# Kernel optimization log

Hardware: AMD Instinct MI355X
Metric: run time of the kernel (lower is better)

The kernel has to match this reference:

```python
import jax, jax.numpy as jnp
import numpy as np

# ---- static dims ----
B, C, T, H, W = 8, 3, 2, 256, 256
P = 16
GH, GW = H // P, W // P          # 16, 16 patch grid
HW = GH * GW                      # 256 patches per frame
D = 512                           # model dim
HEADS, DH = 8, 64
INNER = HEADS * DH                # 512
FF = 4 * D
Q, K, L = 256, 1024, 1            # quant_dim, codebook_size, code_seq_len
DEPTH = 2                         # spatial/temporal depth
CPP = C * P * P                   # 768
SCALE = 1.0 / float(np.sqrt(DH))


def _ln(x, g, b):
    m = jnp.mean(x, -1, keepdims=True)
    v = jnp.mean(jnp.square(x - m), -1, keepdims=True)
    return (x - m) * jax.lax.rsqrt(v + 1e-5) * g + b


def _attn(x, wqkv, wo, bias):
    N, S, _ = x.shape
    q, k, v = jnp.split(x @ wqkv, 3, axis=-1)
    q = q.reshape(N, S, HEADS, DH)
    k = k.reshape(N, S, HEADS, DH)
    v = v.reshape(N, S, HEADS, DH)
    s = jnp.einsum('bihd,bjhd->bhij', q, k) * SCALE
    if bias is not None:
        s = s + bias
    a = jax.nn.softmax(s, -1)
    o = jnp.einsum('bhij,bjhd->bihd', a, v).reshape(N, S, INNER)
    return o @ wo


def _cross(x, ctx, wq, wkv, wo):
    N, S, _ = x.shape
    Lc = ctx.shape[1]
    q = (x @ wq).reshape(N, S, HEADS, DH)
    k, v = jnp.split(ctx @ wkv, 2, axis=-1)
    k = k.reshape(N, Lc, HEADS, DH)
    v = v.reshape(N, Lc, HEADS, DH)
    s = jnp.einsum('bihd,bjhd->bhij', q, k) * SCALE
    a = jax.nn.softmax(s, -1)
    o = jnp.einsum('bhij,bjhd->bihd', a, v).reshape(N, S, INNER)
    return o @ wo


def _self_tf(x, bias, params):
    def step(x, p):
        l1g, l1b, wqkv, wo, l2g, l2b, w1, b1, w2, b2 = p
        x = x + _attn(_ln(x, l1g, l1b), wqkv, wo, bias)
        x = x + jax.nn.gelu(_ln(x, l2g, l2b) @ w1 + b1) @ w2 + b2
        return x, None
    x, _ = jax.lax.scan(step, x, params)
    return x


def _dec_tf(x, bias, ctx, params):
    def step(x, p):
        l1g, l1b, wqkv, wo, cg, cbb, wq, wkv, cwo, l2g, l2b, w1, b1, w2, b2 = p
        x = x + _attn(_ln(x, l1g, l1b), wqkv, wo, bias)
        x = x + _cross(_ln(x, cg, cbb), ctx, wq, wkv, cwo)
        x = x + jax.nn.gelu(_ln(x, l2g, l2b) @ w1 + b1) @ w2 + b2
        return x, None
    x, _ = jax.lax.scan(step, x, params)
    return x


def _cpb(w1, b1, w2, b2):
    # continuous relative position bias over the patch grid -> [HEADS, HW, HW]
    yy, xx = jnp.meshgrid(jnp.arange(GH), jnp.arange(GW), indexing='ij')
    pos = jnp.stack([yy, xx], -1).reshape(HW, 2).astype(jnp.float32)
    rel = pos[:, None] - pos[None, :]
    bias = jax.nn.relu(rel @ w1 + b1) @ w2 + b2
    return jnp.transpose(bias, (2, 0, 1))


def _forward(video, pe_ln1g, pe_ln1b, pe_w, pe_b, pe_ln2g, pe_ln2b,
             cpb_w1, cpb_b1, cpb_w2, cpb_b2,
             es_ln1g, es_ln1b, es_wqkv, es_wo, es_ln2g, es_ln2b, es_w1, es_b1, es_w2, es_b2,
             et_ln1g, et_ln1b, et_wqkv, et_wo, et_ln2g, et_ln2b, et_w1, et_b1, et_w2, et_b2,
             ds_ln1g, ds_ln1b, ds_wqkv, ds_wo, ds_clng, ds_clnb, ds_wq, ds_wkv, ds_cwo,
             ds_ln2g, ds_ln2b, ds_w1, ds_b1, ds_w2, ds_b2,
             vq_inw, vq_inb, codebook, vq_outw, vq_outb, noise,
             px_w, px_b):
    # patch embed: b c t (h p1) (w p2) -> b t h w (c p1 p2), LN -> Linear -> LN
    x = video.reshape(B, C, T, GH, P, GW, P).transpose(0, 2, 3, 5, 1, 4, 6).reshape(B, T, GH, GW, CPP)
    x = _ln(x, pe_ln1g, pe_ln1b) @ pe_w + pe_b
    tokens = _ln(x, pe_ln2g, pe_ln2b)                      # [B, T, GH, GW, D]

    bias = _cpb(cpb_w1, cpb_b1, cpb_w2, cpb_b2)

    # encoder: spatial over (b t)(h w), temporal over (b h w) t
    sp = _self_tf(tokens.reshape(B * T, HW, D), bias,
                  (es_ln1g, es_ln1b, es_wqkv, es_wo, es_ln2g, es_ln2b, es_w1, es_b1, es_w2, es_b2))
    tm = sp.reshape(B, T, GH, GW, D).transpose(0, 2, 3, 1, 4).reshape(B * HW, T, D)
    tm = _self_tf(tm, None,
                  (et_ln1g, et_ln1b, et_wqkv, et_wo, et_ln2g, et_ln2b, et_w1, et_b1, et_w2, et_b2))
    tokens = tm.reshape(B, GH, GW, T, D).transpose(0, 3, 1, 2, 4)  # [B, T, GH, GW, D]

    # NSVQ bottleneck on the last-frame tokens
    feat = tokens[:, 1].reshape(B, HW, D).mean(1)          # [B, D]
    z = (feat @ vq_inw + vq_inb).reshape(B, L, Q)
    d2 = (jnp.sum(z * z, -1, keepdims=True)
          - 2.0 * jnp.einsum('blq,kq->blk', z, codebook)
          + jnp.sum(codebook * codebook, -1))              # [B, L, K]
    idx = jnp.argmin(d2, -1)                               # [B, L]
    hard = codebook[idx]                                   # gather codewords
    err = jnp.linalg.norm(z - hard, axis=-1, keepdims=True)
    zq = z + err / (jnp.linalg.norm(noise, axis=-1, keepdims=True) + 1e-8) * noise
    act = zq @ vq_outw + vq_outb                           # [B, L, D] action tokens

    # decoder: spatial transformer with cross-attn to quantized action tokens
    ctx = jnp.broadcast_to(act[:, None], (B, T, L, D)).reshape(B * T, L, D)
    dec = _dec_tf(tokens.reshape(B * T, HW, D), bias, ctx,
                  (ds_ln1g, ds_ln1b, ds_wqkv, ds_wo, ds_clng, ds_clnb, ds_wq, ds_wkv, ds_cwo,
                   ds_ln2g, ds_ln2b, ds_w1, ds_b1, ds_w2, ds_b2))
    pix = dec.reshape(B, T, GH, GW, D) @ px_w + px_b        # [B, T, GH, GW, CPP]
    recon = pix.reshape(B, T, GH, GW, C, P, P).transpose(0, 4, 1, 2, 5, 3, 6).reshape(B, C, T, H, W)
    return recon


def setup_inputs() -> dict:
    key = jax.random.key(0)
    ks = jax.random.split(key, 64)
    ctr = iter(range(64))
    def nrm(shape, s=0.02):
        return (jax.random.normal(ks[next(ctr)], shape) * s).astype(jnp.float32)
    ones = lambda sh: jnp.ones(sh, jnp.float32)
    zeros = lambda sh: jnp.zeros(sh, jnp.float32)
    inp = dict(
        video=jax.random.normal(ks[next(ctr)], (B, C, T, H, W), jnp.float32),
        pe_ln1g=ones((CPP,)), pe_ln1b=zeros((CPP,)), pe_w=nrm((CPP, D)), pe_b=zeros((D,)),
        pe_ln2g=ones((D,)), pe_ln2b=zeros((D,)),
        cpb_w1=nrm((2, D), 0.1), cpb_b1=zeros((D,)), cpb_w2=nrm((D, HEADS), 0.1), cpb_b2=zeros((HEADS,)),
        es_ln1g=ones((DEPTH, D)), es_ln1b=zeros((DEPTH, D)), es_wqkv=nrm((DEPTH, D, 3 * INNER)),
        es_wo=nrm((DEPTH, INNER, D)), es_ln2g=ones((DEPTH, D)), es_ln2b=zeros((DEPTH, D)),
        es_w1=nrm((DEPTH, D, FF)), es_b1=zeros((DEPTH, FF)), es_w2=nrm((DEPTH, FF, D)), es_b2=zeros((DEPTH, D)),
        et_ln1g=ones((DEPTH, D)), et_ln1b=zeros((DEPTH, D)), et_wqkv=nrm((DEPTH, D, 3 * INNER)),
        et_wo=nrm((DEPTH, INNER, D)), et_ln2g=ones((DEPTH, D)), et_ln2b=zeros((DEPTH, D)),
        et_w1=nrm((DEPTH, D, FF)), et_b1=zeros((DEPTH, FF)), et_w2=nrm((DEPTH, FF, D)), et_b2=zeros((DEPTH, D)),
        ds_ln1g=ones((DEPTH, D)), ds_ln1b=zeros((DEPTH, D)), ds_wqkv=nrm((DEPTH, D, 3 * INNER)),
        ds_wo=nrm((DEPTH, INNER, D)), ds_clng=ones((DEPTH, D)), ds_clnb=zeros((DEPTH, D)),
        ds_wq=nrm((DEPTH, D, INNER)), ds_wkv=nrm((DEPTH, D, 2 * INNER)), ds_cwo=nrm((DEPTH, INNER, D)),
        ds_ln2g=ones((DEPTH, D)), ds_ln2b=zeros((DEPTH, D)),
        ds_w1=nrm((DEPTH, D, FF)), ds_b1=zeros((DEPTH, FF)), ds_w2=nrm((DEPTH, FF, D)), ds_b2=zeros((DEPTH, D)),
        vq_inw=nrm((D, Q)), vq_inb=zeros((Q,)), codebook=nrm((K, Q), 0.05),
        vq_outw=nrm((Q, D)), vq_outb=zeros((D,)),
        noise=jax.random.normal(ks[next(ctr)], (B, L, Q), jnp.float32),
        px_w=nrm((D, CPP)), px_b=zeros((CPP,)),
    )
    return inp


def reference(video, pe_ln1g, pe_ln1b, pe_w, pe_b, pe_ln2g, pe_ln2b,
              cpb_w1, cpb_b1, cpb_w2, cpb_b2,
              es_ln1g, es_ln1b, es_wqkv, es_wo, es_ln2g, es_ln2b, es_w1, es_b1, es_w2, es_b2,
              et_ln1g, et_ln1b, et_wqkv, et_wo, et_ln2g, et_ln2b, et_w1, et_b1, et_w2, et_b2,
              ds_ln1g, ds_ln1b, ds_wqkv, ds_wo, ds_clng, ds_clnb, ds_wq, ds_wkv, ds_cwo,
              ds_ln2g, ds_ln2b, ds_w1, ds_b1, ds_w2, ds_b2,
              vq_inw, vq_inb, codebook, vq_outw, vq_outb, noise,
              px_w, px_b):
    return _forward(video, pe_ln1g, pe_ln1b, pe_w, pe_b, pe_ln2g, pe_ln2b,
                    cpb_w1, cpb_b1, cpb_w2, cpb_b2,
                    es_ln1g, es_ln1b, es_wqkv, es_wo, es_ln2g, es_ln2b, es_w1, es_b1, es_w2, es_b2,
                    et_ln1g, et_ln1b, et_wqkv, et_wo, et_ln2g, et_ln2b, et_w1, et_b1, et_w2, et_b2,
                    ds_ln1g, ds_ln1b, ds_wqkv, ds_wo, ds_clng, ds_clnb, ds_wq, ds_wkv, ds_cwo,
                    ds_ln2g, ds_ln2b, ds_w1, ds_b1, ds_w2, ds_b2,
                    vq_inw, vq_inb, codebook, vq_outw, vq_outb, noise,
                    px_w, px_b)
```

## Files before the change

### kernel.cpp

```cpp
#include <hip/hip_runtime.h>
#include <math.h>

#define SCALE 0.125f

typedef unsigned short u16;
typedef short s16x8 __attribute__((ext_vector_type(8)));
typedef u16 u16x8 __attribute__((ext_vector_type(8)));
typedef float f32x4 __attribute__((ext_vector_type(4)));

__device__ __forceinline__ float wred_sum(float v) {
#pragma unroll
  for (int o = 32; o; o >>= 1) v += __shfl_xor(v, o, 64);
  return v;
}
__device__ __forceinline__ float wred_max(float v) {
#pragma unroll
  for (int o = 32; o; o >>= 1) v = fmaxf(v, __shfl_xor(v, o, 64));
  return v;
}
__device__ __forceinline__ float gelu_tanh(float x) {
  float x3 = x * x * x;
  return 0.5f * x * (1.0f + tanhf(0.7978845608028654f * (x + 0.044715f * x3)));
}
__device__ __forceinline__ u16 f2bf(float f) {
  unsigned u = __float_as_uint(f);
  return (u16)((u + 0x7fffu + ((u >> 16) & 1u)) >> 16);
}

struct TP6 { const float* s0; const float* s1; const float* s2;
             const float* s3; const float* s4; const float* s5; };

__global__ __launch_bounds__(256) void wtrans_k(TP6 p, u16* __restrict__ dst,
                                                int K, int N, size_t mstride) {
  const float* srcs[6] = {p.s0, p.s1, p.s2, p.s3, p.s4, p.s5};
  const float* src = srcs[blockIdx.z];
  u16* d = dst + (size_t)blockIdx.z * mstride;
  __shared__ float t[32][33];
  const int tx = threadIdx.x, ty = threadIdx.y;
  const int n0 = blockIdx.x * 32, k0 = blockIdx.y * 32;
#pragma unroll
  for (int i = 0; i < 4; ++i) t[ty + i * 8][tx] = src[(size_t)(k0 + ty + i * 8) * N + n0 + tx];
  __syncthreads();
#pragma unroll
  for (int i = 0; i < 4; ++i)
    d[(size_t)(n0 + ty + i * 8) * K + k0 + tx] = f2bf(t[tx][ty + i * 8]);
}

template <bool GELU, bool BIAS, bool RES>
__global__ __launch_bounds__(256) void mgemm_k(const float* __restrict__ A,
                                               const u16* __restrict__ Bt,
                                               const float* __restrict__ bias,
                                               const float* __restrict__ res,
                                               float* __restrict__ C,
                                               int M, int N, int K) {
  __shared__ u16 As[128 * 64];
  __shared__ u16 Bs[128 * 64];
  const int tid = threadIdx.x;
  const int lane = tid & 63, wid = tid >> 6;
  const int wr = wid >> 1, wc = wid & 1;
  const int m0 = blockIdx.y * 128, n0 = blockIdx.x * 128;
  f32x4 acc[4][4];
#pragma unroll
  for (int m = 0; m < 4; ++m)
#pragma unroll
    for (int n = 0; n < 4; ++n) acc[m][n] = (f32x4){0.f, 0.f, 0.f, 0.f};

  for (int k0 = 0; k0 < K; k0 += 64) {
#pragma unroll
    for (int p = 0; p < 4; ++p) {
      const int i = p * 256 + tid;
      const int r = i >> 3, c8 = i & 7;
      const float4* src = (const float4*)&A[(size_t)(m0 + r) * K + k0 + c8 * 8];
      const float4 f0 = src[0], f1 = src[1];
      u16x8 h;
      h[0] = f2bf(f0.x); h[1] = f2bf(f0.y); h[2] = f2bf(f0.z); h[3] = f2bf(f0.w);
      h[4] = f2bf(f1.x); h[5] = f2bf(f1.y); h[6] = f2bf(f1.z); h[7] = f2bf(f1.w);
      const int byte = r * 128 + ((c8 * 16) ^ ((r & 7) << 4));
      *(u16x8*)((char*)As + byte) = h;
    }
#pragma unroll
    for (int p = 0; p < 4; ++p) {
      const int i = p * 256 + tid;
      const int r = i >> 3, c = i & 7;
      const u16x8 h = *(const u16x8*)&Bt[(size_t)(n0 + r) * K + k0 + c * 8];
      const int byte = r * 128 + ((c * 16) ^ ((r & 7) << 4));
      *(u16x8*)((char*)Bs + byte) = h;
    }
    __syncthreads();
#pragma unroll
    for (int ks = 0; ks < 2; ++ks) {
      const int kb = ks * 64 + ((lane >> 4) << 4);
      s16x8 af[4], bfr[4];
#pragma unroll
      for (int m = 0; m < 4; ++m) {
        const int r = wr * 64 + m * 16 + (lane & 15);
        af[m] = *(const s16x8*)((const char*)As + r * 128 + (kb ^ ((r & 7) << 4)));
      }
#pragma unroll
      for (int n = 0; n < 4; ++n) {
        const int r = wc * 64 + n * 16 + (lane & 15);
        bfr[n] = *(const s16x8*)((const char*)Bs + r * 128 + (kb ^ ((r & 7) << 4)));
      }
#pragma unroll
      for (int m = 0; m < 4; ++m)
#pragma unroll
        for (int n = 0; n < 4; ++n)
          acc[m][n] = __builtin_amdgcn_mfma_f32_16x16x32_bf16(af[m], bfr[n], acc[m][n], 0, 0, 0);
    }
    __syncthreads();
  }
#pragma unroll
  for (int m = 0; m < 4; ++m) {
    const int row = m0 + wr * 64 + m * 16 + ((lane >> 4) << 2);
#pragma unroll
    for (int n = 0; n < 4; ++n) {
      const int col = n0 + wc * 64 + n * 16 + (lane & 15);
      const float bs = BIAS ? bias[col] : 0.0f;
#pragma unroll
      for (int j = 0; j < 4; ++j) {
        float v = acc[m][n][j] + bs;
        if (GELU) v = gelu_tanh(v);
        if (RES) v += res[(size_t)(row + j) * N + col];
        C[(size_t)(row + j) * N + col] = v;
      }
    }
  }
}

static void mgemm(hipStream_t st, const float* A, const u16* Bt, const float* bias,
                  const float* res, float* C, int M, int N, int K, bool gelu) {
  dim3 g(N / 128, M / 128);
  if (gelu)
    mgemm_k<true, true, false><<<g, 256, 0, st>>>(A, Bt, bias, res, C, M, N, K);
  else if (bias && res)
    mgemm_k<false, true, true><<<g, 256, 0, st>>>(A, Bt, bias, res, C, M, N, K);
  else if (bias)
    mgemm_k<false, true, false><<<g, 256, 0, st>>>(A, Bt, bias, res, C, M, N, K);
  else if (res)
    mgemm_k<false, false, true><<<g, 256, 0, st>>>(A, Bt, bias, res, C, M, N, K);
  else
    mgemm_k<false, false, false><<<g, 256, 0, st>>>(A, Bt, bias, res, C, M, N, K);
}

__global__ __launch_bounds__(256) void pembed_k(const float* __restrict__ video,
                                                const float* __restrict__ g,
                                                const float* __restrict__ b,
                                                float* __restrict__ xpe) {
  const int row = blockIdx.x;
  const int gw_ = row & 15, gh_ = (row >> 4) & 15, t = (row >> 8) & 1, bb = row >> 9;
  const int tid = threadIdx.x;
  float v[3];
  float s = 0.f, ss = 0.f;
#pragma unroll
  for (int r = 0; r < 3; ++r) {
    const int e = tid + r * 256;
    const int c = e >> 8, rem = e & 255, p1 = rem >> 4, p2 = rem & 15;
    v[r] = video[((size_t)(((bb * 3 + c) * 2 + t) * 256 + gh_ * 16 + p1)) * 256 + gw_ * 16 + p2];
    s += v[r];
    ss += v[r] * v[r];
  }
  __shared__ float r1[4], r2[4];
  s = wred_sum(s);
  ss = wred_sum(ss);
  if ((tid & 63) == 0) { r1[tid >> 6] = s; r2[tid >> 6] = ss; }
  __syncthreads();
  const float S = r1[0] + r1[1] + r1[2] + r1[3];
  const float SS = r2[0] + r2[1] + r2[2] + r2[3];
  const float mean = S * (1.0f / 768.0f);
  const float var = SS * (1.0f / 768.0f) - mean * mean;
  const float inv = rsqrtf(var + 1e-5f);
  float* out = xpe + (size_t)row * 768;
#pragma unroll
  for (int r = 0; r < 3; ++r) {
    const int e = tid + r * 256;
    out[e] = (v[r] - mean) * inv * g[e] + b[e];
  }
}

__global__ __launch_bounds__(256) void ln512_k(const float* __restrict__ x,
                                               const float* __restrict__ g,
                                               const float* __restrict__ b,
                                               float* __restrict__ y) {
  const int row = blockIdx.x;
  const int tid = threadIdx.x;
  const float2 v = ((const float2*)(x + (size_t)row * 512))[tid];
  float s = v.x + v.y, ss = v.x * v.x + v.y * v.y;
  __shared__ float r1[4], r2[4];
  s = wred_sum(s);
  ss = wred_sum(ss);
  if ((tid & 63) == 0) { r1[tid >> 6] = s; r2[tid >> 6] = ss; }
  __syncthreads();
  const float S = r1[0] + r1[1] + r1[2] + r1[3];
  const float SS = r2[0] + r2[1] + r2[2] + r2[3];
  const float mean = S * (1.0f / 512.0f);
  const float var = SS * (1.0f / 512.0f) - mean * mean;
  const float inv = rsqrtf(var + 1e-5f);
  const float2 gg = ((const float2*)g)[tid];
  const float2 bb = ((const float2*)b)[tid];
  float2 o;
  o.x = (v.x - mean) * inv * gg.x + bb.x;
  o.y = (v.y - mean) * inv * gg.y + bb.y;
  ((float2*)(y + (size_t)row * 512))[tid] = o;
}

__global__ __launch_bounds__(64) void cpb_k(const float* __restrict__ w1, const float* __restrict__ b1,
                                            const float* __restrict__ w2, const float* __restrict__ b2,
                                            float* __restrict__ table) {
  const int r = blockIdx.x;
  const float ry = (float)(r / 31 - 15), rx = (float)(r % 31 - 15);
  const int lane = threadIdx.x;
  float o[8] = {};
  for (int k = lane; k < 512; k += 64) {
    const float h = fmaxf(ry * w1[k] + rx * w1[512 + k] + b1[k], 0.0f);
#pragma unroll
    for (int j = 0; j < 8; ++j) o[j] += h * w2[k * 8 + j];
  }
#pragma unroll
  for (int j = 0; j < 8; ++j) o[j] = wred_sum(o[j]);
  if (lane == 0)
#pragma unroll
    for (int j = 0; j < 8; ++j) table[r * 8 + j] = o[j] + b2[j];
}

__global__ __launch_bounds__(256) void cpbexpand_k(const float* __restrict__ table,
                                                   float* __restrict__ biasf) {
  const int t = blockIdx.x * 256 + threadIdx.x;
  const int i = t >> 8, j = t & 255;
  const int dy = (i >> 4) - (j >> 4) + 15, dx = (i & 15) - (j & 15) + 15;
  const float* e = table + (dy * 31 + dx) * 8;
#pragma unroll
  for (int h = 0; h < 8; ++h) biasf[(size_t)h * 65536 + t] = e[h];
}

__global__ __launch_bounds__(256) void qk_k(const float* __restrict__ qkv,
                                            const float* __restrict__ biasf,
                                            float* __restrict__ scores) {
  const int bh = blockIdx.z;
  const int n = bh >> 3, h = bh & 7;
  const int i0 = blockIdx.y * 64, j0 = blockIdx.x * 64;
  const float* Qp = qkv + (size_t)n * 256 * 1536 + h * 64;
  const float* Kp = Qp + 512;
  __shared__ float Qs[16][68], Ks[16][68];
  const int tid = threadIdx.x;
  const int tx = tid & 15, ty = tid >> 4;
  float acc[4][4] = {};
  for (int k0 = 0; k0 < 64; k0 += 16) {
    const int rr = tid >> 4, kk = tid & 15;
#pragma unroll
    for (int r = 0; r < 4; ++r) {
      Qs[kk][rr + r * 16] = Qp[(size_t)(i0 + rr + r * 16) * 1536 + k0 + kk];
      Ks[kk][rr + r * 16] = Kp[(size_t)(j0 + rr + r * 16) * 1536 + k0 + kk];
    }
    __syncthreads();
#pragma unroll
    for (int k = 0; k < 16; ++k) {
      const float4 a4 = *(const float4*)&Qs[k][ty * 4];
      const float4 b4 = *(const float4*)&Ks[k][tx * 4];
      const float a[4] = {a4.x, a4.y, a4.z, a4.w};
      const float b[4] = {b4.x, b4.y, b4.z, b4.w};
#pragma unroll
      for (int i = 0; i < 4; ++i)
#pragma unroll
        for (int j = 0; j < 4; ++j) acc[i][j] += a[i] * b[j];
    }
    __syncthreads();
  }
  float* Cp = scores + (size_t)bh * 65536;
#pragma unroll
  for (int i = 0; i < 4; ++i) {
    const int ii = i0 + ty * 4 + i;
#pragma unroll
    for (int j = 0; j < 4; ++j) {
      const int jj = j0 + tx * 4 + j;
      Cp[(size_t)ii * 256 + jj] = acc[i][j] * SCALE + biasf[(size_t)h * 65536 + ii * 256 + jj];
    }
  }
}

__global__ __launch_bounds__(256) void softmax_k(float* __restrict__ scores) {
  const int wid = threadIdx.x >> 6, lane = threadIdx.x & 63;
  const size_t row = (size_t)blockIdx.x * 4 + wid;
  float4 v = ((float4*)(scores + row * 256))[lane];
  float m = fmaxf(fmaxf(v.x, v.y), fmaxf(v.z, v.w));
  m = wred_max(m);
  v.x = expf(v.x - m); v.y = expf(v.y - m); v.z = expf(v.z - m); v.w = expf(v.w - m);
  float s = v.x + v.y + v.z + v.w;
  s = wred_sum(s);
  const float r = 1.0f / s;
  v.x *= r; v.y *= r; v.z *= r; v.w *= r;
  ((float4*)(scores + row * 256))[lane] = v;
}

__global__ __launch_bounds__(256) void pv_k(const float* __restrict__ scores,
                                            const float* __restrict__ qkv,
                                            float* __restrict__ out) {
  const int bh = blockIdx.z;
  const int n = bh >> 3, h = bh & 7;
  const int i0 = blockIdx.y * 64;
  const float* P = scores + (size_t)bh * 65536;
  const float* V = qkv + (size_t)n * 256 * 1536 + 1024 + h * 64;
  __shared__ float Ps[16][68], Vs[16][68];
  const int tid = threadIdx.x;
  const int tx = tid & 15, ty = tid >> 4;
  float acc[4][4] = {};
  for (int k0 = 0; k0 < 256; k0 += 16) {
    const int rr = tid >> 4, kk = tid & 15;
#pragma unroll
    for (int r = 0; r < 4; ++r)
      Ps[kk][rr + r * 16] = P[(size_t)(i0 + rr + r * 16) * 256 + k0 + kk];
    const int kb = tid >> 6, dd = tid & 63;
#pragma unroll
    for (int r = 0; r < 4; ++r)
      Vs[kb + r * 4][dd] = V[(size_t)(k0 + kb + r * 4) * 1536 + dd];
    __syncthreads();
#pragma unroll
    for (int k = 0; k < 16; ++k) {
      const float4 a4 = *(const float4*)&Ps[k][ty * 4];
      const float4 b4 = *(const float4*)&Vs[k][tx * 4];
      const float a[4] = {a4.x, a4.y, a4.z, a4.w};
      const float b[4] = {b4.x, b4.y, b4.z, b4.w};
#pragma unroll
      for (int i = 0; i < 4; ++i)
#pragma unroll
        for (int j = 0; j < 4; ++j) acc[i][j] += a[i] * b[j];
    }
    __syncthreads();
  }
#pragma unroll
  for (int i = 0; i < 4; ++i)
#pragma unroll
    for (int j = 0; j < 4; ++j)
      out[(size_t)(n * 256 + i0 + ty * 4 + i) * 512 + h * 64 + tx * 4 + j] = acc[i][j];
}

__global__ __launch_bounds__(256) void tattn_k(const float* __restrict__ qkv,
                                               float* __restrict__ out) {
  const int wid = threadIdx.x >> 6, lane = threadIdx.x & 63;
  const int idx = blockIdx.x * 4 + wid;
  const int n = idx >> 3, h = idx & 7;
  const float* base = qkv + (size_t)n * 2 * 1536 + h * 64;
  const float q0 = base[lane], q1 = base[1536 + lane];
  const float k0 = base[512 + lane], k1 = base[1536 + 512 + lane];
  const float v0 = base[1024 + lane], v1 = base[1536 + 1024 + lane];
  const float s00 = wred_sum(q0 * k0) * SCALE;
  const float s01 = wred_sum(q0 * k1) * SCALE;
  const float s10 = wred_sum(q1 * k0) * SCALE;
  const float s11 = wred_sum(q1 * k1) * SCALE;
  const float m0 = fmaxf(s00, s01), m1 = fmaxf(s10, s11);
  const float e00 = expf(s00 - m0), e01 = expf(s01 - m0);
  const float e10 = expf(s10 - m1), e11 = expf(s11 - m1);
  const float o0 = (e00 * v0 + e01 * v1) / (e00 + e01);
  const float o1 = (e10 * v0 + e11 * v1) / (e10 + e11);
  out[(size_t)(n * 2 + 0) * 512 + h * 64 + lane] = o0;
  out[(size_t)(n * 2 + 1) * 512 + h * 64 + lane] = o1;
}

__global__ __launch_bounds__(128) void xpose_fwd_k(const float* __restrict__ src, float* __restrict__ dst) {
  const int dr = blockIdx.x;
  const int t = dr & 1, hw = (dr >> 1) & 255, b = dr >> 9;
  const int sr = (b * 2 + t) * 256 + hw;
  ((float4*)(dst + (size_t)dr * 512))[threadIdx.x] = ((const float4*)(src + (size_t)sr * 512))[threadIdx.x];
}
__global__ __launch_bounds__(128) void xpose_bwd_k(const float* __restrict__ src, float* __restrict__ dst) {
  const int dr = blockIdx.x;
  const int hw = dr & 255, t = (dr >> 8) & 1, b = dr >> 9;
  const int sr = (b * 256 + hw) * 2 + t;
  ((float4*)(dst + (size_t)dr * 512))[threadIdx.x] = ((const float4*)(src + (size_t)sr * 512))[threadIdx.x];
}

__global__ __launch_bounds__(256) void featmean_k(const float* __restrict__ x, float* __restrict__ feat) {
  const int b = blockIdx.x, tid = threadIdx.x;
#pragma unroll
  for (int dd = 0; dd < 2; ++dd) {
    const int d = tid + dd * 256;
    float s = 0.f;
    for (int hw = 0; hw < 256; ++hw)
      s += x[(size_t)((b * 2 + 1) * 256 + hw) * 512 + d];
    feat[b * 512 + d] = s * (1.0f / 256.0f);
  }
}

__global__ __launch_bounds__(256) void vecmat_k(const float* __restrict__ A, int lda,
                                                const float* __restrict__ W, int ldw, int coloff,
                                                const float* __restrict__ bias,
                                                float* __restrict__ out, int ldo, int K, int N) {
  const int r = blockIdx.x;
  __shared__ float av[512];
  for (int k = threadIdx.x; k < K; k += 256) av[k] = A[(size_t)r * lda + k];
  __syncthreads();
  for (int n = threadIdx.x; n < N; n += 256) {
    float s = bias ? bias[n] : 0.0f;
    for (int k = 0; k < K; ++k) s += av[k] * W[(size_t)k * ldw + coloff + n];
    out[(size_t)r * ldo + n] = s;
  }
}

__global__ __launch_bounds__(256) void vqargmin_k(const float* __restrict__ z,
                                                  const float* __restrict__ cb,
                                                  float* __restrict__ err_out) {
  const int b = blockIdx.x, tid = threadIdx.x;
  __shared__ float zs[256];
  zs[tid] = z[b * 256 + tid];
  __syncthreads();
  float best = 3.4e38f;
  int bi = 0x7fffffff;
  for (int k = tid; k < 1024; k += 256) {
    float d = 0.f;
    for (int q = 0; q < 256; ++q) {
      const float t = zs[q] - cb[(size_t)k * 256 + q];
      d += t * t;
    }
    if (d < best) { best = d; bi = k; }
  }
  __shared__ float bv[256];
  __shared__ int bix[256];
  bv[tid] = best;
  bix[tid] = bi;
  __syncthreads();
  for (int s = 128; s; s >>= 1) {
    if (tid < s) {
      if (bv[tid + s] < bv[tid] || (bv[tid + s] == bv[tid] && bix[tid + s] < bix[tid])) {
        bv[tid] = bv[tid + s];
        bix[tid] = bix[tid + s];
      }
    }
    __syncthreads();
  }
  const int bk = bix[0];
  __syncthreads();
  const float t = zs[tid] - cb[(size_t)bk * 256 + tid];
  float e = wred_sum(t * t);
  if ((tid & 63) == 0) bv[tid >> 6] = e;
  __syncthreads();
  if (tid == 0) err_out[b] = sqrtf(bv[0] + bv[1] + bv[2] + bv[3]);
}

__global__ __launch_bounds__(256) void zq_k(const float* __restrict__ z,
                                            const float* __restrict__ noise,
                                            const float* __restrict__ err,
                                            float* __restrict__ zq) {
  const int b = blockIdx.x, tid = threadIdx.x;
  const float nv = noise[b * 256 + tid];
  __shared__ float red[4];
  float nn = wred_sum(nv * nv);
  if ((tid & 63) == 0) red[tid >> 6] = nn;
  __syncthreads();
  const float norm = sqrtf(red[0] + red[1] + red[2] + red[3]);
  zq[b * 256 + tid] = z[b * 256 + tid] + err[b] / (norm + 1e-8f) * nv;
}

__global__ __launch_bounds__(128) void bcastadd_k(float* __restrict__ x, const float* __restrict__ u) {
  const int row = blockIdx.x;
  const int b = row >> 9;
  float4* xr = (float4*)(x + (size_t)row * 512);
  const float4 uv = ((const float4*)(u + (size_t)b * 512))[threadIdx.x];
  float4 v = xr[threadIdx.x];
  v.x += uv.x; v.y += uv.y; v.z += uv.z; v.w += uv.w;
  xr[threadIdx.x] = v;
}

__global__ __launch_bounds__(256) void scatter_k(const float* __restrict__ pix, float* __restrict__ out) {
  const int row = blockIdx.x;
  const int gw_ = row & 15, gh_ = (row >> 4) & 15, t = (row >> 8) & 1, bb = row >> 9;
#pragma unroll
  for (int r = 0; r < 3; ++r) {
    const int e = threadIdx.x + r * 256;
    const int c = e >> 8, rem = e & 255, p1 = rem >> 4, p2 = rem & 15;
    out[((size_t)(((bb * 3 + c) * 2 + t) * 256 + gh_ * 16 + p1)) * 256 + gw_ * 16 + p2] =
        pix[(size_t)row * 768 + e];
  }
}

extern "C" void kernel_launch(void* const* d_in, const int* in_sizes, int n_in,
                              void* d_out, int out_size, void* d_ws, size_t ws_size,
                              hipStream_t stream) {
  const float* video   = (const float*)d_in[0];
  const float* pe_ln1g = (const float*)d_in[1];
  const float* pe_ln1b = (const float*)d_in[2];
  const float* pe_w    = (const float*)d_in[3];
  const float* pe_b    = (const float*)d_in[4];
  const float* pe_ln2g = (const float*)d_in[5];
  const float* pe_ln2b = (const float*)d_in[6];
  const float* cpb_w1  = (const float*)d_in[7];
  const float* cpb_b1  = (const float*)d_in[8];
  const float* cpb_w2  = (const float*)d_in[9];
  const float* cpb_b2  = (const float*)d_in[10];
  const float* es_ln1g = (const float*)d_in[11];
  const float* es_ln1b = (const float*)d_in[12];
  const float* es_wqkv = (const float*)d_in[13];
  const float* es_wo   = (const float*)d_in[14];
  const float* es_ln2g = (const float*)d_in[15];
  const float* es_ln2b = (const float*)d_in[16];
  const float* es_w1   = (const float*)d_in[17];
  const float* es_b1   = (const float*)d_in[18];
  const float* es_w2   = (const float*)d_in[19];
  const float* es_b2   = (const float*)d_in[20];
  const float* et_ln1g = (const float*)d_in[21];
  const float* et_ln1b = (const float*)d_in[22];
  const float* et_wqkv = (const float*)d_in[23];
  const float* et_wo   = (const float*)d_in[24];
  const float* et_ln2g = (const float*)d_in[25];
  const float* et_ln2b = (const float*)d_in[26];
  const float* et_w1   = (const float*)d_in[27];
  const float* et_b1   = (const float*)d_in[28];
  const float* et_w2   = (const float*)d_in[29];
  const float* et_b2   = (const float*)d_in[30];
  const float* ds_ln1g = (const float*)d_in[31];
  const float* ds_ln1b = (const float*)d_in[32];
  const float* ds_wqkv = (const float*)d_in[33];
  const float* ds_wo   = (const float*)d_in[34];
  const float* ds_wkv  = (const float*)d_in[38];
  const float* ds_cwo  = (const float*)d_in[39];
  const float* ds_ln2g = (const float*)d_in[40];
  const float* ds_ln2b = (const float*)d_in[41];
  const float* ds_w1   = (const float*)d_in[42];
  const float* ds_b1   = (const float*)d_in[43];
  const float* ds_w2   = (const float*)d_in[44];
  const float* ds_b2   = (const float*)d_in[45];
  const float* vq_inw  = (const float*)d_in[46];
  const float* vq_inb  = (const float*)d_in[47];
  const float* codebook= (const float*)d_in[48];
  const float* vq_outw = (const float*)d_in[49];
  const float* vq_outb = (const float*)d_in[50];
  const float* noise   = (const float*)d_in[51];
  const float* px_w    = (const float*)d_in[52];
  const float* px_b    = (const float*)d_in[53];
  float* out = (float*)d_out;

  float* ws = (float*)d_ws;
  float* xpe  = ws;
  float* x    = xpe + 3145728;
  float* lnb  = x + 2097152;
  float* qkvb = lnb + 2097152;
  float* scr  = qkvb + 6291456;
  float* attn = scr + 8388608;
  float* tmb  = attn + 2097152;
  float* biasf= tmb + 2097152;
  float* table= biasf + 524288;
  float* feat = table + 7688;
  float* zbuf = feat + 4096;
  float* zqb  = zbuf + 2048;
  float* act  = zqb + 2048;
  float* vctx = act + 4096;
  float* ubuf = vctx + 4096;
  float* errb = ubuf + 4096;
  u16* wbf    = (u16*)(errb + 8);
  u16* pe_wt  = wbf;
  u16* qkv_wt = pe_wt + 393216;
  u16* wo_wt  = qkv_wt + 4718592;
  u16* w1_wt  = wo_wt + 1572864;
  u16* w2_wt  = w1_wt + 6291456;
  u16* px_wt  = w2_wt + 6291456;

  const int M = 4096;

  {
    TP6 pqkv = {es_wqkv, es_wqkv + 786432, et_wqkv, et_wqkv + 786432, ds_wqkv, ds_wqkv + 786432};
    wtrans_k<<<dim3(48, 16, 6), dim3(32, 8), 0, stream>>>(pqkv, qkv_wt, 512, 1536, 786432);
    TP6 pwo = {es_wo, es_wo + 262144, et_wo, et_wo + 262144, ds_wo, ds_wo + 262144};
    wtrans_k<<<dim3(16, 16, 6), dim3(32, 8), 0, stream>>>(pwo, wo_wt, 512, 512, 262144);
    TP6 pw1 = {es_w1, es_w1 + 1048576, et_w1, et_w1 + 1048576, ds_w1, ds_w1 + 1048576};
    wtrans_k<<<dim3(64, 16, 6), dim3(32, 8), 0, stream>>>(pw1, w1_wt, 512, 2048, 1048576);
    TP6 pw2 = {es_w2, es_w2 + 1048576, et_w2, et_w2 + 1048576, ds_w2, ds_w2 + 1048576};
    wtrans_k<<<dim3(16, 64, 6), dim3(32, 8), 0, stream>>>(pw2, w2_wt, 2048, 512, 1048576);
    TP6 ppe = {pe_w, pe_w, pe_w, pe_w, pe_w, pe_w};
    wtrans_k<<<dim3(16, 24, 1), dim3(32, 8), 0, stream>>>(ppe, pe_wt, 768, 512, 0);
    TP6 ppx = {px_w, px_w, px_w, px_w, px_w, px_w};
    wtrans_k<<<dim3(24, 16, 1), dim3(32, 8), 0, stream>>>(ppx, px_wt, 512, 768, 0);
  }

  pembed_k<<<4096, 256, 0, stream>>>(video, pe_ln1g, pe_ln1b, xpe);
  mgemm(stream, xpe, pe_wt, pe_b, nullptr, lnb, M, 512, 768, false);
  ln512_k<<<4096, 256, 0, stream>>>(lnb, pe_ln2g, pe_ln2b, x);

  cpb_k<<<961, 64, 0, stream>>>(cpb_w1, cpb_b1, cpb_w2, cpb_b2, table);
  cpbexpand_k<<<256, 256, 0, stream>>>(table, biasf);

  for (int d = 0; d < 2; ++d) {
    const int li = 0 * 2 + d;
    ln512_k<<<4096, 256, 0, stream>>>(x, es_ln1g + d * 512, es_ln1b + d * 512, lnb);
    mgemm(stream, lnb, qkv_wt + (size_t)li * 786432, nullptr, nullptr, qkvb, M, 1536, 512, false);
    qk_k<<<dim3(4, 4, 128), 256, 0, stream>>>(qkvb, biasf, scr);
    softmax_k<<<8192, 256, 0, stream>>>(scr);
    pv_k<<<dim3(1, 4, 128), 256, 0, stream>>>(scr, qkvb, attn);
    mgemm(stream, attn, wo_wt + (size_t)li * 262144, nullptr, x, x, M, 512, 512, false);
    ln512_k<<<4096, 256, 0, stream>>>(x, es_ln2g + d * 512, es_ln2b + d * 512, lnb);
    mgemm(stream, lnb, w1_wt + (size_t)li * 1048576, es_b1 + d * 2048, nullptr, scr, M, 2048, 512, true);
    mgemm(stream, scr, w2_wt + (size_t)li * 1048576, es_b2 + d * 512, x, x, M, 512, 2048, false);
  }

  xpose_fwd_k<<<4096, 128, 0, stream>>>(x, tmb);
  for (int d = 0; d < 2; ++d) {
    const int li = 1 * 2 + d;
    ln512_k<<<4096, 256, 0, stream>>>(tmb, et_ln1g + d * 512, et_ln1b + d * 512, lnb);
    mgemm(stream, lnb, qkv_wt + (size_t)li * 786432, nullptr, nullptr, qkvb, M, 1536, 512, false);
    tattn_k<<<4096, 256, 0, stream>>>(qkvb, attn);
    mgemm(stream, attn, wo_wt + (size_t)li * 262144, nullptr, tmb, tmb, M, 512, 512, false);
    ln512_k<<<4096, 256, 0, stream>>>(tmb, et_ln2g + d * 512, et_ln2b + d * 512, lnb);
    mgemm(stream, lnb, w1_wt + (size_t)li * 1048576, et_b1 + d * 2048, nullptr, scr, M, 2048, 512, true);
    mgemm(stream, scr, w2_wt + (size_t)li * 1048576, et_b2 + d * 512, tmb, tmb, M, 512, 2048, false);
  }
  xpose_bwd_k<<<4096, 128, 0, stream>>>(tmb, x);

  featmean_k<<<8, 256, 0, stream>>>(x, feat);
  vecmat_k<<<8, 256, 0, stream>>>(feat, 512, vq_inw, 256, 0, vq_inb, zbuf, 256, 512, 256);
  vqargmin_k<<<8, 256, 0, stream>>>(zbuf, codebook, errb);
  zq_k<<<8, 256, 0, stream>>>(zbuf, noise, errb, zqb);
  vecmat_k<<<8, 256, 0, stream>>>(zqb, 256, vq_outw, 512, 0, vq_outb, act, 512, 256, 512);

  for (int d = 0; d < 2; ++d) {
    const int li = 2 * 2 + d;
    ln512_k<<<4096, 256, 0, stream>>>(x, ds_ln1g + d * 512, ds_ln1b + d * 512, lnb);
    mgemm(stream, lnb, qkv_wt + (size_t)li * 786432, nullptr, nullptr, qkvb, M, 1536, 512, false);
    qk_k<<<dim3(4, 4, 128), 256, 0, stream>>>(qkvb, biasf, scr);
    softmax_k<<<8192, 256, 0, stream>>>(scr);
    pv_k<<<dim3(1, 4, 128), 256, 0, stream>>>(scr, qkvb, attn);
    mgemm(stream, attn, wo_wt + (size_t)li * 262144, nullptr, x, x, M, 512, 512, false);
    vecmat_k<<<8, 256, 0, stream>>>(act, 512, ds_wkv + (size_t)d * 512 * 1024, 1024, 512, nullptr, vctx, 512, 512, 512);
    vecmat_k<<<8, 256, 0, stream>>>(vctx, 512, ds_cwo + (size_t)d * 512 * 512, 512, 0, nullptr, ubuf, 512, 512, 512);
    bcastadd_k<<<4096, 128, 0, stream>>>(x, ubuf);
    ln512_k<<<4096, 256, 0, stream>>>(x, ds_ln2g + d * 512, ds_ln2b + d * 512, lnb);
    mgemm(stream, lnb, w1_wt + (size_t)li * 1048576, ds_b1 + d * 2048, nullptr, scr, M, 2048, 512, true);
    mgemm(stream, scr, w2_wt + (size_t)li * 1048576, ds_b2 + d * 512, x, x, M, 512, 2048, false);
  }

  mgemm(stream, x, px_wt, px_b, nullptr, xpe, M, 768, 512, false);
  scatter_k<<<4096, 256, 0, stream>>>(xpe, out);
}
```

Before: 2.138 ms.

## Parallelize small VQ and vector-matrix kernels across more blocks and waves

Rewrites the small per-batch kernels (feature mean, vector-matrix products, VQ argmin and noise injection), which previously ran on only 8 blocks with serial inner loops. The feature mean is split over 64 blocks. The vector-matrix product now handles all 8 rows per block, tiling over output columns and splitting K across waves, so each weight element is read once instead of once per row. The VQ argmin and zq kernels are merged into one 1024-thread kernel that uses wave-wide reductions over float4 codebook rows. The aim is to cut the latency of these serialized tail kernels, at the cost of a slightly different tie-breaking order in the argmin.

```diff
diff --git a/kernel.cpp b/kernel.cpp
--- a/kernel.cpp
+++ b/kernel.cpp
@@ -369,84 +369,110 @@
 }
 
 __global__ __launch_bounds__(256) void featmean_k(const float* __restrict__ x, float* __restrict__ feat) {
-  const int b = blockIdx.x, tid = threadIdx.x;
-#pragma unroll
-  for (int dd = 0; dd < 2; ++dd) {
-    const int d = tid + dd * 256;
-    float s = 0.f;
-    for (int hw = 0; hw < 256; ++hw)
-      s += x[(size_t)((b * 2 + 1) * 256 + hw) * 512 + d];
-    feat[b * 512 + d] = s * (1.0f / 256.0f);
-  }
-}
-
-__global__ __launch_bounds__(256) void vecmat_k(const float* __restrict__ A, int lda,
-                                                const float* __restrict__ W, int ldw, int coloff,
-                                                const float* __restrict__ bias,
-                                                float* __restrict__ out, int ldo, int K, int N) {
-  const int r = blockIdx.x;
-  __shared__ float av[512];
-  for (int k = threadIdx.x; k < K; k += 256) av[k] = A[(size_t)r * lda + k];
-  __syncthreads();
-  for (int n = threadIdx.x; n < N; n += 256) {
-    float s = bias ? bias[n] : 0.0f;
-    for (int k = 0; k < K; ++k) s += av[k] * W[(size_t)k * ldw + coloff + n];
-    out[(size_t)r * ldo + n] = s;
-  }
-}
-
-__global__ __launch_bounds__(256) void vqargmin_k(const float* __restrict__ z,
-                                                  const float* __restrict__ cb,
-                                                  float* __restrict__ err_out) {
-  const int b = blockIdx.x, tid = threadIdx.x;
+  const int b = blockIdx.x, d0 = blockIdx.y * 64;
+  const int t = threadIdx.x;
+  const int d = d0 + (t & 63), sl = t >> 6;
+  float s = 0.f;
+#pragma unroll 8
+  for (int i = 0; i < 64; ++i) {
+    const int hw = sl * 64 + i;
+    s += x[(size_t)((b * 2 + 1) * 256 + hw) * 512 + d];
+  }
+  __shared__ float red[4][64];
+  red[sl][t & 63] = s;
+  __syncthreads();
+  if (t < 64)
+    feat[b * 512 + d0 + t] = (red[0][t] + red[1][t] + red[2][t] + red[3][t]) * (1.0f / 256.0f);
+}
+
+template <int K>
+__global__ __launch_bounds__(256) void vecmat8_k(const float* __restrict__ A,
+                                                 const float* __restrict__ W, int ldw, int coloff,
+                                                 const float* __restrict__ bias,
+                                                 float* __restrict__ out, int ldo) {
+  constexpr int KS = K / 4;
+  constexpr int F4R = K / 4;
+  __shared__ float als[8][K];
+  __shared__ float red[4][8][64];
+  const int t = threadIdx.x;
+  const int n0 = blockIdx.x * 64;
+#pragma unroll
+  for (int p = 0; p < (8 * K) / 1024; ++p) {
+    const int i4 = p * 256 + t;
+    const int r = i4 / F4R, c4 = (i4 % F4R) * 4;
+    *(float4*)&als[r][c4] = *(const float4*)&A[(size_t)r * K + c4];
+  }
+  __syncthreads();
+  const int nl = t & 63, sl = t >> 6;
+  const int kb = sl * KS;
+  const float* Wp = W + (size_t)kb * ldw + coloff + n0 + nl;
+  float acc[8] = {};
+#pragma unroll 8
+  for (int kk = 0; kk < KS; ++kk) {
+    const float w = Wp[(size_t)kk * ldw];
+#pragma unroll
+    for (int r = 0; r < 8; ++r) acc[r] = fmaf(als[r][kb + kk], w, acc[r]);
+  }
+#pragma unroll
+  for (int r = 0; r < 8; ++r) red[sl][r][nl] = acc[r];
+  __syncthreads();
+  if (t < 64) {
+    const float bs = bias ? bias[n0 + t] : 0.0f;
+#pragma unroll
+    for (int r = 0; r < 8; ++r) {
+      const float s = red[0][r][t] + red[1][r][t] + red[2][r][t] + red[3][r][t] + bs;
+      out[(size_t)r * ldo + n0 + t] = s;
+    }
+  }
+}
+
+__global__ __launch_bounds__(1024) void vq_k(const float* __restrict__ z,
+                                             const float* __restrict__ cb,
+                                             const float* __restrict__ noise,
+                                             float* __restrict__ zq) {
+  const int b = blockIdx.x;
+  const int t = threadIdx.x, lane = t & 63, wid = t >> 6;
   __shared__ float zs[256];
-  zs[tid] = z[b * 256 + tid];
-  __syncthreads();
-  float best = 3.4e38f;
-  int bi = 0x7fffffff;
-  for (int k = tid; k < 1024; k += 256) {
-    float d = 0.f;
-    for (int q = 0; q < 256; ++q) {
-      const float t = zs[q] - cb[(size_t)k * 256 + q];
-      d += t * t;
-    }
-    if (d < best) { best = d; bi = k; }
-  }
-  __shared__ float bv[256];
-  __shared__ int bix[256];
-  bv[tid] = best;
-  bix[tid] = bi;
-  __syncthreads();
-  for (int s = 128; s; s >>= 1) {
-    if (tid < s) {
-      if (bv[tid + s] < bv[tid] || (bv[tid + s] == bv[tid] && bix[tid + s] < bix[tid])) {
-        bv[tid] = bv[tid + s];
-        bix[tid] = bix[tid + s];
-      }
-    }
-    __syncthreads();
-  }
-  const int bk = bix[0];
-  __syncthreads();
-  const float t = zs[tid] - cb[(size_t)bk * 256 + tid];
-  float e = wred_sum(t * t);
-  if ((tid & 63) == 0) bv[tid >> 6] = e;
-  __syncthreads();
-  if (tid == 0) err_out[b] = sqrtf(bv[0] + bv[1] + bv[2] + bv[3]);
-}
-
-__global__ __launch_bounds__(256) void zq_k(const float* __restrict__ z,
-                                            const float* __restrict__ noise,
-                                            const float* __restrict__ err,
-                                            float* __restrict__ zq) {
-  const int b = blockIdx.x, tid = threadIdx.x;
-  const float nv = noise[b * 256 + tid];
-  __shared__ float red[4];
-  float nn = wred_sum(nv * nv);
-  if ((tid & 63) == 0) red[tid >> 6] = nn;
-  __syncthreads();
-  const float norm = sqrtf(red[0] + red[1] + red[2] + red[3]);
-  zq[b * 256 + tid] = z[b * 256 + tid] + err[b] / (norm + 1e-8f) * nv;
+  __shared__ float wbd[16];
+  __shared__ int wbk[16];
+  __shared__ float esh, nsh;
+  __shared__ int bks;
+  if (t < 256) zs[t] = z[b * 256 + t];
+  __syncthreads();
+  const float4 zl = ((const float4*)zs)[lane];
+  float bd = 3.4e38f;
+  int bk = 0x7fffffff;
+  for (int i = 0; i < 64; ++i) {
+    const int k = wid * 64 + i;
+    const float4 c4 = *(const float4*)&cb[(size_t)k * 256 + lane * 4];
+    const float dx = zl.x - c4.x, dy = zl.y - c4.y, dz = zl.z - c4.z, dw = zl.w - c4.w;
+    float d = dx * dx + dy * dy + dz * dz + dw * dw;
+    d = wred_sum(d);
+    if (d < bd) { bd = d; bk = k; }
+  }
+  if (lane == 0) { wbd[wid] = bd; wbk[wid] = bk; }
+  __syncthreads();
+  if (t == 0) {
+    float best = wbd[0];
+    int bi = wbk[0];
+    for (int w = 1; w < 16; ++w)
+      if (wbd[w] < best) { best = wbd[w]; bi = wbk[w]; }
+    bks = bi;
+  }
+  __syncthreads();
+  const int kbest = bks;
+  if (wid == 0) {
+    const float4 c4 = *(const float4*)&cb[(size_t)kbest * 256 + lane * 4];
+    const float dx = zl.x - c4.x, dy = zl.y - c4.y, dz = zl.z - c4.z, dw = zl.w - c4.w;
+    const float e2 = wred_sum(dx * dx + dy * dy + dz * dz + dw * dw);
+    if (lane == 0) esh = sqrtf(e2);
+  } else if (wid == 1) {
+    const float4 n4 = ((const float4*)(noise + b * 256))[lane];
+    const float nn = wred_sum(n4.x * n4.x + n4.y * n4.y + n4.z * n4.z + n4.w * n4.w);
+    if (lane == 0) nsh = sqrtf(nn);
+  }
+  __syncthreads();
+  if (t < 256) zq[b * 256 + t] = zs[t] + esh / (nsh + 1e-8f) * noise[b * 256 + t];
 }
 
 __global__ __launch_bounds__(128) void bcastadd_k(float* __restrict__ x, const float* __restrict__ u) {
@@ -602,11 +628,10 @@
   }
   xpose_bwd_k<<<4096, 128, 0, stream>>>(tmb, x);
 
-  featmean_k<<<8, 256, 0, stream>>>(x, feat);
-  vecmat_k<<<8, 256, 0, stream>>>(feat, 512, vq_inw, 256, 0, vq_inb, zbuf, 256, 512, 256);
-  vqargmin_k<<<8, 256, 0, stream>>>(zbuf, codebook, errb);
-  zq_k<<<8, 256, 0, stream>>>(zbuf, noise, errb, zqb);
-  vecmat_k<<<8, 256, 0, stream>>>(zqb, 256, vq_outw, 512, 0, vq_outb, act, 512, 256, 512);
+  featmean_k<<<dim3(8, 8), 256, 0, stream>>>(x, feat);
+  vecmat8_k<512><<<4, 256, 0, stream>>>(feat, vq_inw, 256, 0, vq_inb, zbuf, 256);
+  vq_k<<<8, 1024, 0, stream>>>(zbuf, codebook, noise, zqb);
+  vecmat8_k<256><<<8, 256, 0, stream>>>(zqb, vq_outw, 512, 0, vq_outb, act, 512);
 
   for (int d = 0; d < 2; ++d) {
     const int li = 2 * 2 + d;
@@ -616,8 +641,8 @@
     softmax_k<<<8192, 256, 0, stream>>>(scr);
     pv_k<<<dim3(1, 4, 128), 256, 0, stream>>>(scr, qkvb, attn);
     mgemm(stream, attn, wo_wt + (size_t)li * 262144, nullptr, x, x, M, 512, 512, false);
-    vecmat_k<<<8, 256, 0, stream>>>(act, 512, ds_wkv + (size_t)d * 512 * 1024, 1024, 512, nullptr, vctx, 512, 512, 512);
-    vecmat_k<<<8, 256, 0, stream>>>(vctx, 512, ds_cwo + (size_t)d * 512 * 512, 512, 0, nullptr, ubuf, 512, 512, 512);
+    vecmat8_k<512><<<8, 256, 0, stream>>>(act, ds_wkv + (size_t)d * 512 * 1024, 1024, 512, nullptr, vctx, 512);
+    vecmat8_k<512><<<8, 256, 0, stream>>>(vctx, ds_cwo + (size_t)d * 512 * 512, 512, 0, nullptr, ubuf, 512);
     bcastadd_k<<<4096, 128, 0, stream>>>(x, ubuf);
     ln512_k<<<4096, 256, 0, stream>>>(x, ds_ln2g + d * 512, ds_ln2b + d * 512, lnb);
     mgemm(stream, lnb, w1_wt + (size_t)li * 1048576, ds_b1 + d * 2048, nullptr, scr, M, 2048, 512, true);
```

Result: faster. 1.827 ms (-14.5%).
